# Performance work log

Measured on AMD Instinct MI355X. Metric: run time of the kernel, lower is better.

Reference implementation:

```python
import jax, jax.numpy as jnp
import numpy as np

LAMBDA_CE = 1.0
LAMBDA_PROTO = 0.001
FEAT_SCALE = 0.05  # keeps squared distances O(1) so exp(-d2) is non-degenerate


def setup_inputs() -> dict:
    key = jax.random.key(0)
    k1, k2, k3, k4 = jax.random.split(key, 4)
    N, C, P, D = 8192, 32000, 1024, 256
    logits = jax.random.normal(k1, (N, C), dtype=jnp.float32)
    prototypes = jax.random.normal(k2, (P, D), dtype=jnp.float32) * FEAT_SCALE
    features = jax.random.normal(k3, (N, D), dtype=jnp.float32) * FEAT_SCALE
    targets = jax.random.randint(k4, (N,), 0, C, dtype=jnp.int64)
    return {"logits": logits, "prototypes": prototypes, "features": features, "targets": targets}


def reference(logits, prototypes, features, targets):
    # Cross-entropy with mean reduction (nn.CrossEntropyLoss default)
    logp = jax.nn.log_softmax(logits, axis=-1)                  # [N, C]
    ce_loss = -jnp.mean(jnp.take_along_axis(logp, targets[:, None], axis=-1))

    # Gaussian prototype loss: -log(sum_p exp(-||f_n - p||^2)) averaged over n.
    # Squared distance via GEMM expansion instead of the [N, P, D] broadcast.
    f2 = jnp.sum(features * features, axis=-1, keepdims=True)   # [N, 1]
    p2 = jnp.sum(prototypes * prototypes, axis=-1)              # [P]
    d2 = f2 + p2[None, :] - 2.0 * (features @ prototypes.T)     # [N, P]
    proto_loss = -jnp.mean(jnp.log(jnp.sum(jnp.exp(-d2), axis=1)))

    total_loss = LAMBDA_CE * ce_loss + LAMBDA_PROTO * proto_loss
    return (total_loss, ce_loss, proto_loss)
```

## Files before the change

### kernel.cpp

```cpp
#include <hip/hip_runtime.h>
#include <math.h>

#define N_ROWS  8192
#define N_CLS   32000
#define N_PROTO 1024
#define N_DIM   256


__global__ __launch_bounds__(64) void p2_kernel(const float* __restrict__ protos,
                                                float* __restrict__ p2) {
    int c = blockIdx.x;
    int lane = threadIdx.x;
    const float4* pr = (const float4*)(protos + (size_t)c * N_DIM);
    float4 v = pr[lane];
    float s = v.x*v.x + v.y*v.y + v.z*v.z + v.w*v.w;
    #pragma unroll
    for (int off = 32; off > 0; off >>= 1) s += __shfl_down(s, off);
    if (lane == 0) p2[c] = s;
}

__global__ __launch_bounds__(256) void ce_kernel(const float* __restrict__ logits,
                                                 const int* __restrict__ targets,
                                                 float* __restrict__ ce_rows) {
    int row = blockIdx.x;
    int tid = threadIdx.x;
    const float4* rp = (const float4*)(logits + (size_t)row * N_CLS);
    float s = 0.f;
    for (int i = tid; i < N_CLS / 4; i += 256) {
        float4 v = rp[i];
        s += __expf(v.x) + __expf(v.y) + __expf(v.z) + __expf(v.w);
    }
    __shared__ float red[256];
    red[tid] = s;
    __syncthreads();
    #pragma unroll
    for (int off = 128; off > 0; off >>= 1) {
        if (tid < off) red[tid] += red[tid + off];
        __syncthreads();
    }
    if (tid == 0) {
        int tgt = targets[row];
        float xt = logits[(size_t)row * N_CLS + tgt];
        ce_rows[row] = logf(red[0]) - xt;
    }
}

__global__ __launch_bounds__(256) void proto_kernel(const float* __restrict__ feats,
                                                    const float* __restrict__ protos,
                                                    const float* __restrict__ p2,
                                                    float* __restrict__ partial) {
    __shared__ __align__(16) float Fs[32][N_DIM];
    __shared__ float f2s[32];
    __shared__ float wlog[4];

    int tid = threadIdx.x;
    int row0 = blockIdx.x * 32;

    const float4* fv = (const float4*)(feats + (size_t)row0 * N_DIM);
    float4* sv = (float4*)&Fs[0][0];
    for (int i = tid; i < 32 * N_DIM / 4; i += 256) sv[i] = fv[i];
    __syncthreads();

    if (tid < 32) {
        const float4* fr = (const float4*)&Fs[tid][0];
        float a = 0.f;
        for (int d = 0; d < N_DIM / 4; ++d) {
            float4 x = fr[d];
            a += x.x*x.x + x.y*x.y + x.z*x.z + x.w*x.w;
        }
        f2s[tid] = a;
    }
    __syncthreads();

    const int tc = tid & 63;
    const int tr = tid >> 6;
    const int r0 = tr * 8;

    float psum[8] = {0.f, 0.f, 0.f, 0.f, 0.f, 0.f, 0.f, 0.f};

    for (int g = 0; g < 4; ++g) {
        const int cb = g * 256 + tc;
        const float4* pA = (const float4*)(protos + (size_t)(cb      ) * N_DIM);
        const float4* pB = (const float4*)(protos + (size_t)(cb +  64) * N_DIM);
        const float4* pC = (const float4*)(protos + (size_t)(cb + 128) * N_DIM);
        const float4* pD = (const float4*)(protos + (size_t)(cb + 192) * N_DIM);

        float accA[8] = {0,0,0,0,0,0,0,0};
        float accB[8] = {0,0,0,0,0,0,0,0};
        float accC[8] = {0,0,0,0,0,0,0,0};
        float accD[8] = {0,0,0,0,0,0,0,0};

        #pragma unroll 2
        for (int d4 = 0; d4 < N_DIM / 4; ++d4) {
            float4 a = pA[d4], b = pB[d4], c = pC[d4], d = pD[d4];
            #pragma unroll
            for (int r = 0; r < 8; ++r) {
                float4 f = *(const float4*)&Fs[r0 + r][d4 * 4];
                accA[r] += a.x*f.x + a.y*f.y + a.z*f.z + a.w*f.w;
                accB[r] += b.x*f.x + b.y*f.y + b.z*f.z + b.w*f.w;
                accC[r] += c.x*f.x + c.y*f.y + c.z*f.z + c.w*f.w;
                accD[r] += d.x*f.x + d.y*f.y + d.z*f.z + d.w*f.w;
            }
        }
        float p2A = p2[cb], p2B = p2[cb + 64], p2C = p2[cb + 128], p2D = p2[cb + 192];
        #pragma unroll
        for (int r = 0; r < 8; ++r) {
            float f2 = f2s[r0 + r];
            psum[r] += __expf(2.f*accA[r] - f2 - p2A)
                     + __expf(2.f*accB[r] - f2 - p2B)
                     + __expf(2.f*accC[r] - f2 - p2C)
                     + __expf(2.f*accD[r] - f2 - p2D);
        }
    }

    float lsum = 0.f;
    #pragma unroll
    for (int r = 0; r < 8; ++r) {
        float v = psum[r];
        #pragma unroll
        for (int off = 32; off > 0; off >>= 1) v += __shfl_down(v, off);
        if (tc == 0) lsum += logf(v);
    }
    if (tc == 0) wlog[tr] = lsum;
    __syncthreads();
    if (tid == 0) partial[blockIdx.x] = wlog[0] + wlog[1] + wlog[2] + wlog[3];
}

__global__ __launch_bounds__(256) void finalize_kernel(const float* __restrict__ ws,
                                                       float* __restrict__ out) {
    int tid = threadIdx.x;
    float ce = 0.f;
    for (int i = tid; i < N_ROWS; i += 256) ce += ws[i];
    float pl = ws[N_ROWS + tid];
    __shared__ float r1[256], r2[256];
    r1[tid] = ce; r2[tid] = pl;
    __syncthreads();
    #pragma unroll
    for (int off = 128; off > 0; off >>= 1) {
        if (tid < off) { r1[tid] += r1[tid + off]; r2[tid] += r2[tid + off]; }
        __syncthreads();
    }
    if (tid == 0) {
        float ce_mean = r1[0] / (float)N_ROWS;
        float proto_loss = -r2[0] / (float)N_ROWS;
        out[0] = 1.0f * ce_mean + 0.001f * proto_loss;
        out[1] = ce_mean;
        out[2] = proto_loss;
    }
}

extern "C" void kernel_launch(void* const* d_in, const int* in_sizes, int n_in,
                              void* d_out, int out_size, void* d_ws, size_t ws_size,
                              hipStream_t stream) {
    const float* logits  = (const float*)d_in[0];
    const float* protos  = (const float*)d_in[1];
    const float* feats   = (const float*)d_in[2];
    const int*   targets = (const int*)d_in[3];
    float* out = (float*)d_out;
    float* ws  = (float*)d_ws;

    float* ce_rows    = ws;
    float* proto_part = ws + N_ROWS;
    float* p2         = ws + N_ROWS + 256;

    hipLaunchKernelGGL(p2_kernel,       dim3(N_PROTO), dim3(64),  0, stream, protos, p2);
    hipLaunchKernelGGL(ce_kernel,       dim3(N_ROWS),  dim3(256), 0, stream, logits, targets, ce_rows);
    hipLaunchKernelGGL(proto_kernel,    dim3(N_ROWS/32), dim3(256), 0, stream, feats, protos, p2, proto_part);
    hipLaunchKernelGGL(finalize_kernel, dim3(1),       dim3(256), 0, stream, ws, out);
}
```

Baseline: 1.528 ms.

## Stage prototype tiles in swizzled LDS and unroll CE loads with nontemporal hints

The proto kernel now loads 64-prototype tiles cooperatively into a new 64 KB shared-memory buffer with an XOR swizzle, replacing the per-thread strided global loads of whole prototype rows. The per-thread accumulator set drops from 32 to 8, and the kernel syncs once per tile. The CE kernel issues four independent nontemporal float4 loads per iteration into separate accumulators to raise memory-level parallelism on the logits stream. In exchange, the larger LDS footprint (about 97 KB per block) limits occupancy and the extra tile barriers add synchronisation.

```diff
diff --git a/kernel.cpp b/kernel.cpp
--- a/kernel.cpp
+++ b/kernel.cpp
@@ -5,6 +5,11 @@
 #define N_CLS   32000
 #define N_PROTO 1024
 #define N_DIM   256
+
+#define PTILE   64
+#define NTILES  (N_PROTO / PTILE)
+
+typedef float f32x4 __attribute__((ext_vector_type(4)));
 
 
 __global__ __launch_bounds__(64) void p2_kernel(const float* __restrict__ protos,
@@ -24,12 +29,24 @@
                                                  float* __restrict__ ce_rows) {
     int row = blockIdx.x;
     int tid = threadIdx.x;
-    const float4* rp = (const float4*)(logits + (size_t)row * N_CLS);
-    float s = 0.f;
-    for (int i = tid; i < N_CLS / 4; i += 256) {
-        float4 v = rp[i];
-        s += __expf(v.x) + __expf(v.y) + __expf(v.z) + __expf(v.w);
+    const f32x4* rp = (const f32x4*)(logits + (size_t)row * N_CLS);
+    float s0 = 0.f, s1 = 0.f, s2 = 0.f, s3 = 0.f;
+    int i = tid;
+    for (; i + 768 < N_CLS / 4; i += 1024) {
+        f32x4 a = __builtin_nontemporal_load(rp + i);
+        f32x4 b = __builtin_nontemporal_load(rp + i + 256);
+        f32x4 c = __builtin_nontemporal_load(rp + i + 512);
+        f32x4 d = __builtin_nontemporal_load(rp + i + 768);
+        s0 += __expf(a.x) + __expf(a.y) + __expf(a.z) + __expf(a.w);
+        s1 += __expf(b.x) + __expf(b.y) + __expf(b.z) + __expf(b.w);
+        s2 += __expf(c.x) + __expf(c.y) + __expf(c.z) + __expf(c.w);
+        s3 += __expf(d.x) + __expf(d.y) + __expf(d.z) + __expf(d.w);
     }
+    for (; i < N_CLS / 4; i += 256) {
+        f32x4 a = __builtin_nontemporal_load(rp + i);
+        s0 += __expf(a.x) + __expf(a.y) + __expf(a.z) + __expf(a.w);
+    }
+    float s = (s0 + s1) + (s2 + s3);
     __shared__ float red[256];
     red[tid] = s;
     __syncthreads();
@@ -50,66 +67,62 @@
                                                     const float* __restrict__ p2,
                                                     float* __restrict__ partial) {
     __shared__ __align__(16) float Fs[32][N_DIM];
+    __shared__ __align__(16) float Ps[PTILE * N_DIM];
     __shared__ float f2s[32];
     __shared__ float wlog[4];
 
     int tid = threadIdx.x;
     int row0 = blockIdx.x * 32;
 
-    const float4* fv = (const float4*)(feats + (size_t)row0 * N_DIM);
-    float4* sv = (float4*)&Fs[0][0];
+    const f32x4* fv = (const f32x4*)(feats + (size_t)row0 * N_DIM);
+    f32x4* sv = (f32x4*)&Fs[0][0];
     for (int i = tid; i < 32 * N_DIM / 4; i += 256) sv[i] = fv[i];
     __syncthreads();
 
     if (tid < 32) {
-        const float4* fr = (const float4*)&Fs[tid][0];
+        const f32x4* fr = (const f32x4*)&Fs[tid][0];
         float a = 0.f;
+        #pragma unroll
         for (int d = 0; d < N_DIM / 4; ++d) {
-            float4 x = fr[d];
+            f32x4 x = fr[d];
             a += x.x*x.x + x.y*x.y + x.z*x.z + x.w*x.w;
         }
         f2s[tid] = a;
     }
-    __syncthreads();
 
     const int tc = tid & 63;
     const int tr = tid >> 6;
     const int r0 = tr * 8;
 
+    f32x4* Ps4 = (f32x4*)Ps;
     float psum[8] = {0.f, 0.f, 0.f, 0.f, 0.f, 0.f, 0.f, 0.f};
 
-    for (int g = 0; g < 4; ++g) {
-        const int cb = g * 256 + tc;
-        const float4* pA = (const float4*)(protos + (size_t)(cb      ) * N_DIM);
-        const float4* pB = (const float4*)(protos + (size_t)(cb +  64) * N_DIM);
-        const float4* pC = (const float4*)(protos + (size_t)(cb + 128) * N_DIM);
-        const float4* pD = (const float4*)(protos + (size_t)(cb + 192) * N_DIM);
+    for (int g = 0; g < NTILES; ++g) {
+        __syncthreads();
+        const f32x4* pg = (const f32x4*)(protos + (size_t)g * PTILE * N_DIM);
+        #pragma unroll
+        for (int j = tid; j < PTILE * N_DIM / 4; j += 256) {
+            f32x4 v = pg[j];
+            int prow = j >> 6;
+            int pcol = j & 63;
+            Ps4[prow * 64 + (pcol ^ (prow & 7))] = v;
+        }
+        __syncthreads();
 
-        float accA[8] = {0,0,0,0,0,0,0,0};
-        float accB[8] = {0,0,0,0,0,0,0,0};
-        float accC[8] = {0,0,0,0,0,0,0,0};
-        float accD[8] = {0,0,0,0,0,0,0,0};
-
-        #pragma unroll 2
+        float acc[8] = {0,0,0,0,0,0,0,0};
+        #pragma unroll 4
         for (int d4 = 0; d4 < N_DIM / 4; ++d4) {
-            float4 a = pA[d4], b = pB[d4], c = pC[d4], d = pD[d4];
+            f32x4 p = Ps4[tc * 64 + (d4 ^ (tc & 7))];
             #pragma unroll
             for (int r = 0; r < 8; ++r) {
-                float4 f = *(const float4*)&Fs[r0 + r][d4 * 4];
-                accA[r] += a.x*f.x + a.y*f.y + a.z*f.z + a.w*f.w;
-                accB[r] += b.x*f.x + b.y*f.y + b.z*f.z + b.w*f.w;
-                accC[r] += c.x*f.x + c.y*f.y + c.z*f.z + c.w*f.w;
-                accD[r] += d.x*f.x + d.y*f.y + d.z*f.z + d.w*f.w;
+                f32x4 f = *(const f32x4*)&Fs[r0 + r][d4 * 4];
+                acc[r] += p.x*f.x + p.y*f.y + p.z*f.z + p.w*f.w;
             }
         }
-        float p2A = p2[cb], p2B = p2[cb + 64], p2C = p2[cb + 128], p2D = p2[cb + 192];
+        float p2v = p2[g * PTILE + tc];
         #pragma unroll
         for (int r = 0; r < 8; ++r) {
-            float f2 = f2s[r0 + r];
-            psum[r] += __expf(2.f*accA[r] - f2 - p2A)
-                     + __expf(2.f*accB[r] - f2 - p2B)
-                     + __expf(2.f*accC[r] - f2 - p2C)
-                     + __expf(2.f*accD[r] - f2 - p2D);
+            psum[r] += __expf(2.f*acc[r] - f2s[r0 + r] - p2v);
         }
     }
 
@@ -163,8 +176,8 @@
     float* proto_part = ws + N_ROWS;
     float* p2         = ws + N_ROWS + 256;
 
-    hipLaunchKernelGGL(p2_kernel,       dim3(N_PROTO), dim3(64),  0, stream, protos, p2);
-    hipLaunchKernelGGL(ce_kernel,       dim3(N_ROWS),  dim3(256), 0, stream, logits, targets, ce_rows);
+    hipLaunchKernelGGL(p2_kernel,       dim3(N_PROTO),   dim3(64),  0, stream, protos, p2);
+    hipLaunchKernelGGL(ce_kernel,       dim3(N_ROWS),    dim3(256), 0, stream, logits, targets, ce_rows);
     hipLaunchKernelGGL(proto_kernel,    dim3(N_ROWS/32), dim3(256), 0, stream, feats, protos, p2, proto_part);
-    hipLaunchKernelGGL(finalize_kernel, dim3(1),       dim3(256), 0, stream, ws, out);
+    hipLaunchKernelGGL(finalize_kernel, dim3(1),         dim3(256), 0, stream, ws, out);
 }
```

After: 1.459 ms. 4.5% less time.
